# Optimization experiments

Measured on AMD Instinct MI355X. Metric: run time of the kernel, lower is better.

## Reference

```python
import jax, jax.numpy as jnp
import numpy as np
import math

def setup_inputs() -> dict:
    key = jax.random.key(0)
    k1, k2, k3 = jax.random.split(key, 3)
    B, S, E = 2, 2048, 1024
    H, D = 16, 64
    inputs = jax.random.normal(k1, (B, S, E), dtype=jnp.float32)
    Wqkv = jax.random.uniform(k2, (E, 3 * H * D), minval=-0.1, maxval=0.1, dtype=jnp.float32)
    Wo = jax.random.uniform(k3, (H * D, E), minval=-0.1, maxval=0.1, dtype=jnp.float32)
    return {"inputs": inputs, "Wqkv": Wqkv, "Wo": Wo, "nhead": H}

def reference(inputs, Wqkv, Wo, nhead):
    B, S, E = inputs.shape
    H = int(nhead)
    D = Wqkv.shape[1] // (3 * H)
    causal, ghost = True, True

    qkv = jnp.matmul(inputs, Wqkv)                       # (B, S, 3*H*D)
    qkv = qkv.reshape(B, S, 3, H, D)
    Q = qkv[:, :, 0].transpose(0, 2, 1, 3)               # (B, H, S, D)
    K = qkv[:, :, 1].transpose(0, 2, 1, 3)
    V = qkv[:, :, 2].transpose(0, 2, 1, 3)

    scores = jnp.einsum('bhqd,bhkd->bhqk', Q, K) / math.sqrt(D)
    if causal:
        neg_inf = jnp.float32(-jnp.inf)
        mask = jnp.where(jnp.triu(jnp.ones((S, S), dtype=bool), k=1), neg_inf, jnp.float32(0.0))
        scores = scores + mask  # broadcast over (B, H)

    # ghost softmax: standard stable softmax but denominator gets +1
    z = jnp.exp(scores - jnp.max(scores, axis=-1, keepdims=True))
    denom = jnp.sum(z, axis=-1, keepdims=True)
    if ghost:
        denom = denom + jnp.float32(1.0)
    attn = z / denom                                      # (B, H, S, S)

    A = jnp.einsum('bhqk,bhkd->bhqd', attn, V)            # (B, H, S, D)
    A = A.transpose(0, 2, 1, 3).reshape(B, S, H * D)      # (B, S, H*D)
    return jnp.matmul(A, Wo)
```

## Files before the change

### kernel.cpp

```cpp
#include <hip/hip_runtime.h>

typedef float    f32x4  __attribute__((ext_vector_type(4)));
typedef _Float16 half8  __attribute__((ext_vector_type(8)));
typedef _Float16 half4v __attribute__((ext_vector_type(4)));

#define MFMA16(a,b,c) __builtin_amdgcn_mfma_f32_16x16x32_f16(a,b,c,0,0,0)

__device__ __forceinline__ float exp2_fast(float x){
  float y; asm("v_exp_f32 %0, %1" : "=v"(y) : "v"(x)); return y;
}
__device__ __forceinline__ void gload_lds16(const _Float16* g, _Float16* l){
  __builtin_amdgcn_global_load_lds(
      (const __attribute__((address_space(1))) unsigned int*)(g),
      (__attribute__((address_space(3))) unsigned int*)(l),
      16, 0, 0);
}

#define S_LEN 2048
#define E_DIM 1024
#define H_NUM 16
#define D_DIM 64
#define NBH   32
#define M_ROWS 4096
#define N3    3072
#define LOG2E 1.44269504089f

__global__ void cast_x_kernel(const float* __restrict__ in,
                              _Float16* __restrict__ hi, int n4){
  int i = blockIdx.x * 256 + threadIdx.x;
  if (i >= n4) return;
  const float4 v = reinterpret_cast<const float4*>(in)[i];
  half4v h;
  h[0] = (_Float16)v.x; h[1] = (_Float16)v.y;
  h[2] = (_Float16)v.z; h[3] = (_Float16)v.w;
  *reinterpret_cast<half4v*>(&hi[i*4]) = h;
}

__global__ void transpose_half(const float* __restrict__ in,
                               _Float16* __restrict__ hi, int R, int C){
  __shared__ float tile[32][33];
  int bx = blockIdx.x * 32, by = blockIdx.y * 32;
  int tx = threadIdx.x & 31, ty = threadIdx.x >> 5;
#pragma unroll
  for (int i = ty; i < 32; i += 8)
    tile[i][tx] = in[(size_t)(by + i) * C + bx + tx];
  __syncthreads();
#pragma unroll
  for (int i = ty; i < 32; i += 8)
    hi[(size_t)(bx + i) * R + by + tx] = (_Float16)tile[tx][i];
}

template<int EPI>
__global__ __launch_bounds__(256, 3) void gemm97(
    const _Float16* __restrict__ A, const _Float16* __restrict__ B,
    int Kdim, int Ndim, float* __restrict__ Cout,
    _Float16* __restrict__ qh, _Float16* __restrict__ kh, _Float16* __restrict__ vh)
{
  __shared__ __align__(16) _Float16 sA[128][64], sB[128][64];
  const int tid = threadIdx.x;
  const int m0 = blockIdx.y * 128, n0 = blockIdx.x * 128;
  const int wid = tid >> 6, lane = tid & 63;
  const int wr = (wid >> 1) * 64, wc = (wid & 1) * 64;
  const int lr = lane & 15, lc = lane >> 4;
  const int ldrow = lane >> 3;
  const int ldcol = ((lane & 7) ^ ldrow) * 8;
  const int swz = (lr & 7) << 4;

  f32x4 acc[4][4] = {};
  const int nK = Kdim >> 6;
  for (int ks = 0; ks < nK; ++ks){
    const int k0 = ks << 6;
#pragma unroll
    for (int cc = 0; cc < 4; ++cc){
      const int c = wid * 4 + cc;
      const int row = c * 8 + ldrow;
      gload_lds16(&A[(size_t)(m0 + row) * Kdim + k0 + ldcol], &sA[c*8][0]);
      gload_lds16(&B[(size_t)(n0 + row) * Kdim + k0 + ldcol], &sB[c*8][0]);
    }
    __syncthreads();
    const char* ab = (const char*)&sA[0][0];
    const char* bb = (const char*)&sB[0][0];
#pragma unroll
    for (int kk = 0; kk < 64; kk += 32){
      half8 fa[4], fb[4];
#pragma unroll
      for (int t = 0; t < 4; ++t){
        fa[t] = *reinterpret_cast<const half8*>(
            ab + (wr + t*16 + lr)*128 + ((kk*2 + lc*16) ^ swz));
        fb[t] = *reinterpret_cast<const half8*>(
            bb + (wc + t*16 + lr)*128 + ((kk*2 + lc*16) ^ swz));
      }
#pragma unroll
      for (int mt = 0; mt < 4; ++mt)
#pragma unroll
        for (int nt = 0; nt < 4; ++nt)
          acc[mt][nt] = MFMA16(fa[mt], fb[nt], acc[mt][nt]);
    }
    __syncthreads();
  }
#pragma unroll
  for (int mt = 0; mt < 4; ++mt)
#pragma unroll
    for (int nt = 0; nt < 4; ++nt)
#pragma unroll
      for (int r = 0; r < 4; ++r){
        const int m = m0 + wr + mt*16 + lc*4 + r;
        const int n = n0 + wc + nt*16 + lr;
        float v = acc[mt][nt][r];
        if (EPI == 0){
          Cout[(size_t)m * Ndim + n] = v;
        } else {
          const int t = n >> 10, rem = n & 1023, hh = rem >> 6, d = rem & 63;
          const int b = m >> 11, s = m & 2047;
          const int bh = b * H_NUM + hh;
          if (t == 0) v *= (0.125f * LOG2E);
          size_t o;
          if (t == 2)  o = ((size_t)bh * D_DIM + d) * S_LEN + s;
          else         o = ((size_t)bh * S_LEN + s) * D_DIM + d;
          _Float16* ph = (t == 0) ? qh : (t == 1) ? kh : vh;
          ph[o] = (_Float16)v;
        }
      }
}

__global__ __launch_bounds__(256, 4) void gemm64(
    const _Float16* __restrict__ A, const _Float16* __restrict__ B,
    int Kdim, int Ndim, float* __restrict__ Cout)
{
  __shared__ __align__(16) _Float16 sA[64][64], sB[128][64];
  const int tid = threadIdx.x;
  const int m0 = blockIdx.y * 64, n0 = blockIdx.x * 128;
  const int wid = tid >> 6, lane = tid & 63;
  const int wr = (wid >> 1) * 32, wc = (wid & 1) * 64;
  const int lr = lane & 15, lc = lane >> 4;
  const int ldrow = lane >> 3;
  const int ldcol = ((lane & 7) ^ ldrow) * 8;
  const int swz = (lr & 7) << 4;

  f32x4 acc[2][4] = {};
  const int nK = Kdim >> 6;
  for (int ks = 0; ks < nK; ++ks){
    const int k0 = ks << 6;
#pragma unroll
    for (int cc = 0; cc < 2; ++cc){
      const int c = wid * 2 + cc;
      const int row = c * 8 + ldrow;
      gload_lds16(&A[(size_t)(m0 + row) * Kdim + k0 + ldcol], &sA[c*8][0]);
    }
#pragma unroll
    for (int cc = 0; cc < 4; ++cc){
      const int c = wid * 4 + cc;
      const int row = c * 8 + ldrow;
      gload_lds16(&B[(size_t)(n0 + row) * Kdim + k0 + ldcol], &sB[c*8][0]);
    }
    __syncthreads();
    const char* ab = (const char*)&sA[0][0];
    const char* bb = (const char*)&sB[0][0];
#pragma unroll
    for (int kk = 0; kk < 64; kk += 32){
      half8 fa[2], fb[4];
#pragma unroll
      for (int t = 0; t < 2; ++t)
        fa[t] = *reinterpret_cast<const half8*>(
            ab + (wr + t*16 + lr)*128 + ((kk*2 + lc*16) ^ swz));
#pragma unroll
      for (int t = 0; t < 4; ++t)
        fb[t] = *reinterpret_cast<const half8*>(
            bb + (wc + t*16 + lr)*128 + ((kk*2 + lc*16) ^ swz));
#pragma unroll
      for (int mt = 0; mt < 2; ++mt)
#pragma unroll
        for (int nt = 0; nt < 4; ++nt)
          acc[mt][nt] = MFMA16(fa[mt], fb[nt], acc[mt][nt]);
    }
    __syncthreads();
  }
#pragma unroll
  for (int mt = 0; mt < 2; ++mt)
#pragma unroll
    for (int nt = 0; nt < 4; ++nt)
#pragma unroll
      for (int r = 0; r < 4; ++r){
        const int m = m0 + wr + mt*16 + lc*4 + r;
        const int n = n0 + wc + nt*16 + lr;
        Cout[(size_t)m * Ndim + n] = acc[mt][nt][r];
      }
}

__global__ __launch_bounds__(256, 4) void attn_kernel(
    const _Float16* __restrict__ Qh, const _Float16* __restrict__ Kh,
    const _Float16* __restrict__ Vth, _Float16* __restrict__ Ao)
{
  __shared__ __align__(16) _Float16 sK[2][64][64];
  __shared__ __align__(16) _Float16 sV[64][64];
  __shared__ __align__(16) _Float16 sP[4][16][64];
  const int tid = threadIdx.x, wid = tid >> 6, lane = tid & 63;
  const int id  = blockIdx.x + 32 * blockIdx.y;
  const int xcd = id & 7, seq = id >> 3;
  const int bh  = xcd + 8 * (seq & 3);
  const int g = seq >> 2, hsel = g & 7, bsel = g >> 3;
  const int qt = (bsel == 0) ? 31 - hsel
               : (bsel == 1) ? hsel
               : (bsel == 2) ? 23 - hsel
                             : 8 + hsel;
  const int q0 = qt * 64;
  const int nT = qt + 1;
  const int lr = lane & 15, lc = lane >> 4;
  const int swz = (lr & 7) << 4;
  const size_t base = (size_t)bh * S_LEN * D_DIM;

  const int lrow = lane >> 3;
  const int cswz = ((lane & 7) ^ lrow) * 8;

  auto stageK = [&](int t, int b){
    const int kv0 = t * 64;
#pragma unroll
    for (int cc = 0; cc < 2; ++cc){
      const int c = wid * 2 + cc;
      const int row = c * 8 + lrow;
      gload_lds16(&Kh[base + (size_t)(kv0 + row) * D_DIM + cswz], &sK[b][c*8][0]);
    }
  };
  auto stageV = [&](int t){
    const int kv0 = t * 64;
#pragma unroll
    for (int cc = 0; cc < 2; ++cc){
      const int c = wid * 2 + cc;
      const int row = c * 8 + lrow;
      gload_lds16(&Vth[base + (size_t)row * S_LEN + kv0 + cswz], &sV[c*8][0]);
    }
  };

  const int b = bh >> 4, hh = bh & 15;

  half8 fq[2];
  {
    const int qrow = q0 + wid*16 + lr;
#pragma unroll
    for (int kc = 0; kc < 2; ++kc)
      fq[kc] = *reinterpret_cast<const half8*>(&Qh[base + (size_t)qrow * 64 + kc*32 + lc*8]);
  }

  f32x4 acc[4] = {};
  float m = -1e30f, l = 0.f, tm = -1e30f;

  stageK(0, 0);
  __syncthreads();

  int cur = 0;
  for (int t = 0; t < nT; ++t){
    stageV(t);
    if (t + 1 < nT) stageK(t + 1, cur ^ 1);

    const char* kb = (const char*)&sK[cur][0][0];
    f32x4 sc[4];
    __builtin_amdgcn_s_setprio(1);
#pragma unroll
    for (int nt = 0; nt < 4; ++nt){
      f32x4 z = {};
#pragma unroll
      for (int kc = 0; kc < 2; ++kc){
        const half8 fk = *reinterpret_cast<const half8*>(
            kb + (nt*16 + lr)*128 + ((kc*64 + lc*16) ^ swz));
        z = MFMA16(fk, fq[kc], z);
      }
      sc[nt] = z;
    }
    __builtin_amdgcn_s_setprio(0);

    if (t == qt){
#pragma unroll
      for (int nt = 0; nt < 4; ++nt)
#pragma unroll
        for (int r = 0; r < 4; ++r)
          if (nt*16 + lc*4 + r > wid*16 + lr) sc[nt][r] = -1e30f;
    }

    f32x4 a;
#pragma unroll
    for (int j = 0; j < 4; ++j)
      a[j] = fmaxf(fmaxf(sc[0][j], sc[1][j]), fmaxf(sc[2][j], sc[3][j]));
    float mx = fmaxf(fmaxf(a[0], a[1]), fmaxf(a[2], a[3]));
    mx = fmaxf(mx, __shfl_xor(mx, 16));
    mx = fmaxf(mx, __shfl_xor(mx, 32));
    tm = fmaxf(tm, mx);

    if (__any(mx > m + 8.0f)){
      const float mn = fmaxf(m, mx);
      const float s = exp2_fast(m - mn);
      l *= s; m = mn;
      float rs[4];
#pragma unroll
      for (int r = 0; r < 4; ++r)
        rs[r] = __shfl(s, (lc << 4) | (lc*4 + r), 64);
#pragma unroll
      for (int dt = 0; dt < 4; ++dt)
#pragma unroll
        for (int r = 0; r < 4; ++r) acc[dt][r] *= rs[r];
    }

    f32x4 ssum = {};
#pragma unroll
    for (int nt = 0; nt < 4; ++nt){
#pragma unroll
      for (int r = 0; r < 4; ++r) sc[nt][r] = exp2_fast(sc[nt][r] - m);
      ssum += sc[nt];
    }
    float s1 = (ssum[0] + ssum[1]) + (ssum[2] + ssum[3]);
    s1 += __shfl_xor(s1, 16);
    s1 += __shfl_xor(s1, 32);
    l += s1;

    char* pw = (char*)&sP[wid][0][0];
#pragma unroll
    for (int nt = 0; nt < 4; ++nt){
      int2 pk;
      pk.x = __builtin_bit_cast(int, __builtin_amdgcn_cvt_pkrtz(sc[nt][0], sc[nt][1]));
      pk.y = __builtin_bit_cast(int, __builtin_amdgcn_cvt_pkrtz(sc[nt][2], sc[nt][3]));
      *reinterpret_cast<int2*>(pw + lr*128 + ((nt*32 + lc*8) ^ swz)) = pk;
    }

    const half8 pa0 = *reinterpret_cast<const half8*>(pw + lr*128 + ((lc*16) ^ swz));
    const half8 pa1 = *reinterpret_cast<const half8*>(pw + lr*128 + ((64 + lc*16) ^ swz));

    if (t + 1 < nT) asm volatile("s_waitcnt vmcnt(2)" ::: "memory");
    else            asm volatile("s_waitcnt vmcnt(0)" ::: "memory");
    __builtin_amdgcn_sched_barrier(0);
    __builtin_amdgcn_s_barrier();

    const char* vb = (const char*)&sV[0][0];
    __builtin_amdgcn_s_setprio(1);
#pragma unroll
    for (int dt = 0; dt < 4; ++dt){
#pragma unroll
      for (int kc = 0; kc < 2; ++kc){
        const half8 fv = *reinterpret_cast<const half8*>(
            vb + (dt*16 + lr)*128 + ((kc*64 + lc*16) ^ swz));
        acc[dt] = MFMA16(kc ? pa1 : pa0, fv, acc[dt]);
      }
    }
    __builtin_amdgcn_s_setprio(0);

    __syncthreads();
    cur ^= 1;
  }

  const float den = l + exp2_fast(tm - m);
  float rden[4];
#pragma unroll
  for (int r = 0; r < 4; ++r)
    rden[r] = __shfl(den, (lc << 4) | (lc*4 + r), 64);
#pragma unroll
  for (int dt = 0; dt < 4; ++dt)
#pragma unroll
    for (int r = 0; r < 4; ++r){
      const float o = acc[dt][r] / rden[r];
      const int q = q0 + wid*16 + lc*4 + r;
      const int d = dt*16 + lr;
      Ao[((size_t)(b*S_LEN + q)) * E_DIM + hh*D_DIM + d] = (_Float16)o;
    }
}

extern "C" void kernel_launch(void* const* d_in, const int* in_sizes, int n_in,
                              void* d_out, int out_size, void* d_ws, size_t ws_size,
                              hipStream_t stream){
  const float* X    = (const float*)d_in[0];
  const float* Wqkv = (const float*)d_in[1];
  const float* Wo   = (const float*)d_in[2];
  float* out = (float*)d_out;

  _Float16* w = (_Float16*)d_ws;
  size_t off = 0;
  auto alloc = [&](size_t n){ _Float16* p = w + off; off += n; return p; };
  const size_t ME   = (size_t)M_ROWS * E_DIM;
  const size_t WQ   = (size_t)N3 * E_DIM;
  const size_t WOsz = (size_t)E_DIM * E_DIM;
  const size_t QK   = (size_t)NBH * S_LEN * D_DIM;
  _Float16 *Xh = alloc(ME);
  _Float16 *Wqh = alloc(WQ);
  _Float16 *Woh = alloc(WOsz);
  _Float16 *Qh = alloc(QK), *Kh = alloc(QK), *Vth = alloc(QK);
  _Float16 *Ahalf = alloc(ME);

  cast_x_kernel<<<(int)(ME/4/256), 256, 0, stream>>>(X, Xh, (int)(ME/4));
  transpose_half<<<dim3(N3/32, E_DIM/32), 256, 0, stream>>>(Wqkv, Wqh, E_DIM, N3);
  transpose_half<<<dim3(E_DIM/32, E_DIM/32), 256, 0, stream>>>(Wo, Woh, E_DIM, E_DIM);

  gemm97<1><<<dim3(N3/128, M_ROWS/128), 256, 0, stream>>>(
      Xh, Wqh, E_DIM, N3, nullptr, Qh, Kh, Vth);

  attn_kernel<<<dim3(32, NBH), 256, 0, stream>>>(Qh, Kh, Vth, Ahalf);

  gemm64<<<dim3(E_DIM/128, M_ROWS/64), 256, 0, stream>>>(
      Ahalf, Woh, E_DIM, E_DIM, out);
}
```

Before: 119.4 us.

## Restructure attention to 2-wave blocks processing paired 32-row query tiles

The attention kernel moves from 256-thread blocks handling one 64-row query tile to 128-thread blocks that each handle two 32-row query tiles, paired as a heavy tile and a light tile (63-p and p), so causal work is balanced per block. The K/V double buffer and prefetch pipeline are removed. Each iteration now loads K and V together, waits for all loads, and synchronizes before compute. This cuts LDS usage and should raise occupancy, but it gives up overlap of global loads with compute. It also reloads each KV tile for every 32 query rows instead of every 64, doubling KV traffic.

```diff
diff --git a/kernel.cpp b/kernel.cpp
--- a/kernel.cpp
+++ b/kernel.cpp
@@ -187,24 +187,18 @@
       }
 }
 
-__global__ __launch_bounds__(256, 4) void attn_kernel(
+__global__ __launch_bounds__(128, 4) void attn_kernel(
     const _Float16* __restrict__ Qh, const _Float16* __restrict__ Kh,
     const _Float16* __restrict__ Vth, _Float16* __restrict__ Ao)
 {
-  __shared__ __align__(16) _Float16 sK[2][64][64];
+  __shared__ __align__(16) _Float16 sK[64][64];
   __shared__ __align__(16) _Float16 sV[64][64];
-  __shared__ __align__(16) _Float16 sP[4][16][64];
+  __shared__ __align__(16) _Float16 sP[2][16][64];
   const int tid = threadIdx.x, wid = tid >> 6, lane = tid & 63;
-  const int id  = blockIdx.x + 32 * blockIdx.y;
+  const int id  = blockIdx.x;
   const int xcd = id & 7, seq = id >> 3;
   const int bh  = xcd + 8 * (seq & 3);
-  const int g = seq >> 2, hsel = g & 7, bsel = g >> 3;
-  const int qt = (bsel == 0) ? 31 - hsel
-               : (bsel == 1) ? hsel
-               : (bsel == 2) ? 23 - hsel
-                             : 8 + hsel;
-  const int q0 = qt * 64;
-  const int nT = qt + 1;
+  const int p   = seq >> 2;
   const int lr = lane & 15, lc = lane >> 4;
   const int swz = (lr & 7) << 4;
   const size_t base = (size_t)bh * S_LEN * D_DIM;
@@ -212,153 +206,143 @@
   const int lrow = lane >> 3;
   const int cswz = ((lane & 7) ^ lrow) * 8;
 
-  auto stageK = [&](int t, int b){
+  auto stage = [&](int t){
     const int kv0 = t * 64;
 #pragma unroll
-    for (int cc = 0; cc < 2; ++cc){
-      const int c = wid * 2 + cc;
+    for (int cc = 0; cc < 4; ++cc){
+      const int c = wid * 4 + cc;
       const int row = c * 8 + lrow;
-      gload_lds16(&Kh[base + (size_t)(kv0 + row) * D_DIM + cswz], &sK[b][c*8][0]);
+      gload_lds16(&Kh[base + (size_t)(kv0 + row) * D_DIM + cswz], &sK[c*8][0]);
+      gload_lds16(&Vth[base + (size_t)row * S_LEN + kv0 + cswz], &sV[c*8][0]);
     }
   };
-  auto stageV = [&](int t){
-    const int kv0 = t * 64;
-#pragma unroll
-    for (int cc = 0; cc < 2; ++cc){
-      const int c = wid * 2 + cc;
-      const int row = c * 8 + lrow;
-      gload_lds16(&Vth[base + (size_t)row * S_LEN + kv0 + cswz], &sV[c*8][0]);
-    }
-  };
 
   const int b = bh >> 4, hh = bh & 15;
 
-  half8 fq[2];
-  {
-    const int qrow = q0 + wid*16 + lr;
-#pragma unroll
-    for (int kc = 0; kc < 2; ++kc)
-      fq[kc] = *reinterpret_cast<const half8*>(&Qh[base + (size_t)qrow * 64 + kc*32 + lc*8]);
+#pragma unroll 1
+  for (int half = 0; half < 2; ++half){
+    const int a = half ? p : (63 - p);
+    const int q0 = a * 32;
+    const int nT = (a >> 1) + 1;
+
+    half8 fq[2];
+    {
+      const int qrow = q0 + wid*16 + lr;
+#pragma unroll
+      for (int kc = 0; kc < 2; ++kc)
+        fq[kc] = *reinterpret_cast<const half8*>(&Qh[base + (size_t)qrow * 64 + kc*32 + lc*8]);
+    }
+
+    f32x4 acc[4] = {};
+    float m = -1e30f, l = 0.f, tm = -1e30f;
+
+#pragma unroll 1
+    for (int t = 0; t < nT; ++t){
+      __syncthreads();
+      stage(t);
+      asm volatile("s_waitcnt vmcnt(0)" ::: "memory");
+      __syncthreads();
+
+      const char* kb = (const char*)&sK[0][0];
+      f32x4 sc[4];
+      __builtin_amdgcn_s_setprio(1);
+#pragma unroll
+      for (int nt = 0; nt < 4; ++nt){
+        f32x4 z = {};
+#pragma unroll
+        for (int kc = 0; kc < 2; ++kc){
+          const half8 fk = *reinterpret_cast<const half8*>(
+              kb + (nt*16 + lr)*128 + ((kc*64 + lc*16) ^ swz));
+          z = MFMA16(fk, fq[kc], z);
+        }
+        sc[nt] = z;
+      }
+      __builtin_amdgcn_s_setprio(0);
+
+      if (t == nT - 1){
+        const int qg = q0 + wid*16 + lr;
+#pragma unroll
+        for (int nt = 0; nt < 4; ++nt)
+#pragma unroll
+          for (int r = 0; r < 4; ++r)
+            if (t*64 + nt*16 + lc*4 + r > qg) sc[nt][r] = -1e30f;
+      }
+
+      f32x4 aa;
+#pragma unroll
+      for (int j = 0; j < 4; ++j)
+        aa[j] = fmaxf(fmaxf(sc[0][j], sc[1][j]), fmaxf(sc[2][j], sc[3][j]));
+      float mx = fmaxf(fmaxf(aa[0], aa[1]), fmaxf(aa[2], aa[3]));
+      mx = fmaxf(mx, __shfl_xor(mx, 16));
+      mx = fmaxf(mx, __shfl_xor(mx, 32));
+      tm = fmaxf(tm, mx);
+
+      if (__any(mx > m + 8.0f)){
+        const float mn = fmaxf(m, mx);
+        const float s = exp2_fast(m - mn);
+        l *= s; m = mn;
+        float rs[4];
+#pragma unroll
+        for (int r = 0; r < 4; ++r)
+          rs[r] = __shfl(s, (lc << 4) | (lc*4 + r), 64);
+#pragma unroll
+        for (int dt = 0; dt < 4; ++dt)
+#pragma unroll
+          for (int r = 0; r < 4; ++r) acc[dt][r] *= rs[r];
+      }
+
+      f32x4 ssum = {};
+#pragma unroll
+      for (int nt = 0; nt < 4; ++nt){
+#pragma unroll
+        for (int r = 0; r < 4; ++r) sc[nt][r] = exp2_fast(sc[nt][r] - m);
+        ssum += sc[nt];
+      }
+      float s1 = (ssum[0] + ssum[1]) + (ssum[2] + ssum[3]);
+      s1 += __shfl_xor(s1, 16);
+      s1 += __shfl_xor(s1, 32);
+      l += s1;
+
+      char* pw = (char*)&sP[wid][0][0];
+#pragma unroll
+      for (int nt = 0; nt < 4; ++nt){
+        int2 pk;
+        pk.x = __builtin_bit_cast(int, __builtin_amdgcn_cvt_pkrtz(sc[nt][0], sc[nt][1]));
+        pk.y = __builtin_bit_cast(int, __builtin_amdgcn_cvt_pkrtz(sc[nt][2], sc[nt][3]));
+        *reinterpret_cast<int2*>(pw + lr*128 + ((nt*32 + lc*8) ^ swz)) = pk;
+      }
+
+      const half8 pa0 = *reinterpret_cast<const half8*>(pw + lr*128 + ((lc*16) ^ swz));
+      const half8 pa1 = *reinterpret_cast<const half8*>(pw + lr*128 + ((64 + lc*16) ^ swz));
+      const char* vb = (const char*)&sV[0][0];
+      __builtin_amdgcn_s_setprio(1);
+#pragma unroll
+      for (int dt = 0; dt < 4; ++dt){
+#pragma unroll
+        for (int kc = 0; kc < 2; ++kc){
+          const half8 fv = *reinterpret_cast<const half8*>(
+              vb + (dt*16 + lr)*128 + ((kc*64 + lc*16) ^ swz));
+          acc[dt] = MFMA16(kc ? pa1 : pa0, fv, acc[dt]);
+        }
+      }
+      __builtin_amdgcn_s_setprio(0);
+    }
+
+    const float den = l + exp2_fast(tm - m);
+    float rden[4];
+#pragma unroll
+    for (int r = 0; r < 4; ++r)
+      rden[r] = __shfl(den, (lc << 4) | (lc*4 + r), 64);
+#pragma unroll
+    for (int dt = 0; dt < 4; ++dt)
+#pragma unroll
+      for (int r = 0; r < 4; ++r){
+        const float o = acc[dt][r] / rden[r];
+        const int q = q0 + wid*16 + lc*4 + r;
+        const int d = dt*16 + lr;
+        Ao[((size_t)(b*S_LEN + q)) * E_DIM + hh*D_DIM + d] = (_Float16)o;
+      }
   }
-
-  f32x4 acc[4] = {};
-  float m = -1e30f, l = 0.f, tm = -1e30f;
-
-  stageK(0, 0);
-  __syncthreads();
-
-  int cur = 0;
-  for (int t = 0; t < nT; ++t){
-    stageV(t);
-    if (t + 1 < nT) stageK(t + 1, cur ^ 1);
-
-    const char* kb = (const char*)&sK[cur][0][0];
-    f32x4 sc[4];
-    __builtin_amdgcn_s_setprio(1);
-#pragma unroll
-    for (int nt = 0; nt < 4; ++nt){
-      f32x4 z = {};
-#pragma unroll
-      for (int kc = 0; kc < 2; ++kc){
-        const half8 fk = *reinterpret_cast<const half8*>(
-            kb + (nt*16 + lr)*128 + ((kc*64 + lc*16) ^ swz));
-        z = MFMA16(fk, fq[kc], z);
-      }
-      sc[nt] = z;
-    }
-    __builtin_amdgcn_s_setprio(0);
-
-    if (t == qt){
-#pragma unroll
-      for (int nt = 0; nt < 4; ++nt)
-#pragma unroll
-        for (int r = 0; r < 4; ++r)
-          if (nt*16 + lc*4 + r > wid*16 + lr) sc[nt][r] = -1e30f;
-    }
-
-    f32x4 a;
-#pragma unroll
-    for (int j = 0; j < 4; ++j)
-      a[j] = fmaxf(fmaxf(sc[0][j], sc[1][j]), fmaxf(sc[2][j], sc[3][j]));
-    float mx = fmaxf(fmaxf(a[0], a[1]), fmaxf(a[2], a[3]));
-    mx = fmaxf(mx, __shfl_xor(mx, 16));
-    mx = fmaxf(mx, __shfl_xor(mx, 32));
-    tm = fmaxf(tm, mx);
-
-    if (__any(mx > m + 8.0f)){
-      const float mn = fmaxf(m, mx);
-      const float s = exp2_fast(m - mn);
-      l *= s; m = mn;
-      float rs[4];
-#pragma unroll
-      for (int r = 0; r < 4; ++r)
-        rs[r] = __shfl(s, (lc << 4) | (lc*4 + r), 64);
-#pragma unroll
-      for (int dt = 0; dt < 4; ++dt)
-#pragma unroll
-        for (int r = 0; r < 4; ++r) acc[dt][r] *= rs[r];
-    }
-
-    f32x4 ssum = {};
-#pragma unroll
-    for (int nt = 0; nt < 4; ++nt){
-#pragma unroll
-      for (int r = 0; r < 4; ++r) sc[nt][r] = exp2_fast(sc[nt][r] - m);
-      ssum += sc[nt];
-    }
-    float s1 = (ssum[0] + ssum[1]) + (ssum[2] + ssum[3]);
-    s1 += __shfl_xor(s1, 16);
-    s1 += __shfl_xor(s1, 32);
-    l += s1;
-
-    char* pw = (char*)&sP[wid][0][0];
-#pragma unroll
-    for (int nt = 0; nt < 4; ++nt){
-      int2 pk;
-      pk.x = __builtin_bit_cast(int, __builtin_amdgcn_cvt_pkrtz(sc[nt][0], sc[nt][1]));
-      pk.y = __builtin_bit_cast(int, __builtin_amdgcn_cvt_pkrtz(sc[nt][2], sc[nt][3]));
-      *reinterpret_cast<int2*>(pw + lr*128 + ((nt*32 + lc*8) ^ swz)) = pk;
-    }
-
-    const half8 pa0 = *reinterpret_cast<const half8*>(pw + lr*128 + ((lc*16) ^ swz));
-    const half8 pa1 = *reinterpret_cast<const half8*>(pw + lr*128 + ((64 + lc*16) ^ swz));
-
-    if (t + 1 < nT) asm volatile("s_waitcnt vmcnt(2)" ::: "memory");
-    else            asm volatile("s_waitcnt vmcnt(0)" ::: "memory");
-    __builtin_amdgcn_sched_barrier(0);
-    __builtin_amdgcn_s_barrier();
-
-    const char* vb = (const char*)&sV[0][0];
-    __builtin_amdgcn_s_setprio(1);
-#pragma unroll
-    for (int dt = 0; dt < 4; ++dt){
-#pragma unroll
-      for (int kc = 0; kc < 2; ++kc){
-        const half8 fv = *reinterpret_cast<const half8*>(
-            vb + (dt*16 + lr)*128 + ((kc*64 + lc*16) ^ swz));
-        acc[dt] = MFMA16(kc ? pa1 : pa0, fv, acc[dt]);
-      }
-    }
-    __builtin_amdgcn_s_setprio(0);
-
-    __syncthreads();
-    cur ^= 1;
-  }
-
-  const float den = l + exp2_fast(tm - m);
-  float rden[4];
-#pragma unroll
-  for (int r = 0; r < 4; ++r)
-    rden[r] = __shfl(den, (lc << 4) | (lc*4 + r), 64);
-#pragma unroll
-  for (int dt = 0; dt < 4; ++dt)
-#pragma unroll
-    for (int r = 0; r < 4; ++r){
-      const float o = acc[dt][r] / rden[r];
-      const int q = q0 + wid*16 + lc*4 + r;
-      const int d = dt*16 + lr;
-      Ao[((size_t)(b*S_LEN + q)) * E_DIM + hh*D_DIM + d] = (_Float16)o;
-    }
 }
 
 extern "C" void kernel_launch(void* const* d_in, const int* in_sizes, int n_in,
@@ -389,7 +373,7 @@
   gemm97<1><<<dim3(N3/128, M_ROWS/128), 256, 0, stream>>>(
       Xh, Wqh, E_DIM, N3, nullptr, Qh, Kh, Vth);
 
-  attn_kernel<<<dim3(32, NBH), 256, 0, stream>>>(Qh, Kh, Vth, Ahalf);
+  attn_kernel<<<dim3(1024), 128, 0, stream>>>(Qh, Kh, Vth, Ahalf);
 
   gemm64<<<dim3(E_DIM/128, M_ROWS/64), 256, 0, stream>>>(
       Ahalf, Woh, E_DIM, E_DIM, out);
```

After: 127.7 us. +7.0%, slower.

## Split causal attention KV range into two partials and merge in a separate kernel

Applied to the files above, without the earlier changes.

Each query tile's KV loop is divided into two halves handled by separate blocks, doubling the grid to 2048 blocks. Each block writes unnormalized fp16 partial outputs plus running max, sum and ghost term to workspace. A new merge kernel then combines the two halves with softmax rescaling and writes the final normalized attention output. This aims to balance load across the causal triangle and raise occupancy. In exchange it adds a second launch, extra global traffic for the partials, and a loss of precision from storing unnormalized accumulators in fp16.

```diff
diff --git a/kernel.cpp b/kernel.cpp
--- a/kernel.cpp
+++ b/kernel.cpp
@@ -187,27 +187,46 @@
       }
 }
 
-__global__ __launch_bounds__(256, 4) void attn_kernel(
+__global__ __launch_bounds__(256, 4) void attn_partial(
     const _Float16* __restrict__ Qh, const _Float16* __restrict__ Kh,
-    const _Float16* __restrict__ Vth, _Float16* __restrict__ Ao)
+    const _Float16* __restrict__ Vth,
+    _Float16* __restrict__ Opart, float* __restrict__ Spart)
 {
   __shared__ __align__(16) _Float16 sK[2][64][64];
   __shared__ __align__(16) _Float16 sV[64][64];
   __shared__ __align__(16) _Float16 sP[4][16][64];
   const int tid = threadIdx.x, wid = tid >> 6, lane = tid & 63;
-  const int id  = blockIdx.x + 32 * blockIdx.y;
+  const int id  = blockIdx.x;
   const int xcd = id & 7, seq = id >> 3;
   const int bh  = xcd + 8 * (seq & 3);
-  const int g = seq >> 2, hsel = g & 7, bsel = g >> 3;
-  const int qt = (bsel == 0) ? 31 - hsel
-               : (bsel == 1) ? hsel
-               : (bsel == 2) ? 23 - hsel
-                             : 8 + hsel;
+  const int rest = seq >> 2;
+  const int qt  = 31 - (rest >> 1);
+  const int half = rest & 1;
+  const int h0 = (qt + 1) >> 1;
+  const int t0 = half ? h0 : 0;
+  const int t1 = half ? (qt + 1) : h0;
   const int q0 = qt * 64;
-  const int nT = qt + 1;
   const int lr = lane & 15, lc = lane >> 4;
   const int swz = (lr & 7) << 4;
   const size_t base = (size_t)bh * S_LEN * D_DIM;
+
+  const int pidx = (bh * 32 + qt) * 2 + half;
+  _Float16* Op = Opart + (size_t)pidx * 4096;
+  float*    Sp = Spart + (size_t)pidx * 192;
+
+  if (t1 <= t0){
+#pragma unroll
+    for (int dt = 0; dt < 4; ++dt)
+#pragma unroll
+      for (int r = 0; r < 4; ++r)
+        Op[(wid*16 + lc*4 + r)*64 + dt*16 + lr] = (_Float16)0.f;
+    if (lane < 16){
+      Sp[wid*16 + lr] = -1e30f;
+      Sp[64 + wid*16 + lr] = 0.f;
+      Sp[128 + wid*16 + lr] = -1e30f;
+    }
+    return;
+  }
 
   const int lrow = lane >> 3;
   const int cswz = ((lane & 7) ^ lrow) * 8;
@@ -231,8 +250,6 @@
     }
   };
 
-  const int b = bh >> 4, hh = bh & 15;
-
   half8 fq[2];
   {
     const int qrow = q0 + wid*16 + lr;
@@ -244,13 +261,13 @@
   f32x4 acc[4] = {};
   float m = -1e30f, l = 0.f, tm = -1e30f;
 
-  stageK(0, 0);
+  stageK(t0, 0);
   __syncthreads();
 
   int cur = 0;
-  for (int t = 0; t < nT; ++t){
+  for (int t = t0; t < t1; ++t){
     stageV(t);
-    if (t + 1 < nT) stageK(t + 1, cur ^ 1);
+    if (t + 1 < t1) stageK(t + 1, cur ^ 1);
 
     const char* kb = (const char*)&sK[cur][0][0];
     f32x4 sc[4];
@@ -323,7 +340,7 @@
     const half8 pa0 = *reinterpret_cast<const half8*>(pw + lr*128 + ((lc*16) ^ swz));
     const half8 pa1 = *reinterpret_cast<const half8*>(pw + lr*128 + ((64 + lc*16) ^ swz));
 
-    if (t + 1 < nT) asm volatile("s_waitcnt vmcnt(2)" ::: "memory");
+    if (t + 1 < t1) asm volatile("s_waitcnt vmcnt(2)" ::: "memory");
     else            asm volatile("s_waitcnt vmcnt(0)" ::: "memory");
     __builtin_amdgcn_sched_barrier(0);
     __builtin_amdgcn_s_barrier();
@@ -345,20 +362,49 @@
     cur ^= 1;
   }
 
-  const float den = l + exp2_fast(tm - m);
-  float rden[4];
-#pragma unroll
-  for (int r = 0; r < 4; ++r)
-    rden[r] = __shfl(den, (lc << 4) | (lc*4 + r), 64);
 #pragma unroll
   for (int dt = 0; dt < 4; ++dt)
 #pragma unroll
-    for (int r = 0; r < 4; ++r){
-      const float o = acc[dt][r] / rden[r];
-      const int q = q0 + wid*16 + lc*4 + r;
-      const int d = dt*16 + lr;
-      Ao[((size_t)(b*S_LEN + q)) * E_DIM + hh*D_DIM + d] = (_Float16)o;
-    }
+    for (int r = 0; r < 4; ++r)
+      Op[(wid*16 + lc*4 + r)*64 + dt*16 + lr] = (_Float16)acc[dt][r];
+  if (lane < 16){
+    Sp[wid*16 + lr] = m;
+    Sp[64 + wid*16 + lr] = l;
+    Sp[128 + wid*16 + lr] = tm;
+  }
+}
+
+__global__ __launch_bounds__(256) void attn_merge(
+    const _Float16* __restrict__ Opart, const float* __restrict__ Spart,
+    _Float16* __restrict__ Ao)
+{
+  const int id = blockIdx.x;
+  const int bh = id >> 5, qt = id & 31;
+  const int tid = threadIdx.x;
+  const int row = tid >> 2, seg = tid & 3;
+  const int p0 = (bh * 32 + qt) * 2, p1 = p0 + 1;
+  const float* S1 = Spart + (size_t)p0 * 192;
+  const float* S2 = Spart + (size_t)p1 * 192;
+  const float m1 = S1[row], l1 = S1[64 + row], t1 = S1[128 + row];
+  const float m2 = S2[row], l2 = S2[64 + row], t2 = S2[128 + row];
+  const float M  = fmaxf(m1, m2);
+  const float w1 = exp2_fast(m1 - M), w2 = exp2_fast(m2 - M);
+  const float den = l1 * w1 + l2 * w2 + exp2_fast(fmaxf(t1, t2) - M);
+  const float inv = 1.0f / den;
+  const half8* O1 = reinterpret_cast<const half8*>(Opart + (size_t)p0 * 4096 + row * 64 + seg * 16);
+  const half8* O2 = reinterpret_cast<const half8*>(Opart + (size_t)p1 * 4096 + row * 64 + seg * 16);
+  const int b = bh >> 4, hh = bh & 15;
+  const int q = qt * 64 + row;
+  _Float16* dst = Ao + ((size_t)(b * S_LEN + q)) * E_DIM + hh * D_DIM + seg * 16;
+#pragma unroll
+  for (int v = 0; v < 2; ++v){
+    const half8 a1 = O1[v], a2 = O2[v];
+    half8 o;
+#pragma unroll
+    for (int j = 0; j < 8; ++j)
+      o[j] = (_Float16)(((float)a1[j] * w1 + (float)a2[j] * w2) * inv);
+    reinterpret_cast<half8*>(dst)[v] = o;
+  }
 }
 
 extern "C" void kernel_launch(void* const* d_in, const int* in_sizes, int n_in,
@@ -381,6 +427,9 @@
   _Float16 *Woh = alloc(WOsz);
   _Float16 *Qh = alloc(QK), *Kh = alloc(QK), *Vth = alloc(QK);
   _Float16 *Ahalf = alloc(ME);
+  _Float16 *Opart = alloc((size_t)2048 * 4096);
+  _Float16 *Sraw  = alloc((size_t)2048 * 192 * 2);
+  float* Spart = (float*)Sraw;
 
   cast_x_kernel<<<(int)(ME/4/256), 256, 0, stream>>>(X, Xh, (int)(ME/4));
   transpose_half<<<dim3(N3/32, E_DIM/32), 256, 0, stream>>>(Wqkv, Wqh, E_DIM, N3);
@@ -389,7 +438,8 @@
   gemm97<1><<<dim3(N3/128, M_ROWS/128), 256, 0, stream>>>(
       Xh, Wqh, E_DIM, N3, nullptr, Qh, Kh, Vth);
 
-  attn_kernel<<<dim3(32, NBH), 256, 0, stream>>>(Qh, Kh, Vth, Ahalf);
+  attn_partial<<<dim3(2048), 256, 0, stream>>>(Qh, Kh, Vth, Opart, Spart);
+  attn_merge<<<dim3(1024), 256, 0, stream>>>(Opart, Spart, Ahalf);
 
   gemm64<<<dim3(E_DIM/128, M_ROWS/64), 256, 0, stream>>>(
       Ahalf, Woh, E_DIM, E_DIM, out);
```

Measured after the change: 120.9 us. Within noise of the previous version (+1.2%).
